# Kernel tuning notes

Hardware: AMD Instinct MI355X
Metric: run time of the kernel (lower is better)

## Reference

```python
import jax, jax.numpy as jnp
import numpy as np


def setup_inputs() -> dict:
    key = jax.random.key(0)
    k1, k2 = jax.random.split(key)
    z = jax.random.normal(k1, (16, 256, 32, 32), dtype=jnp.float32)
    emb = jax.random.normal(k2, (8192, 256), dtype=jnp.float32)
    return {"z": z, "emb": emb}


def reference(z, emb):
    B, C, H, W = z.shape
    # [B,C,H,W] -> [B*H*W, C], distances in fp32 for precision
    z_f = jnp.transpose(z, (0, 2, 3, 1)).reshape(-1, C).astype(jnp.float32)
    e = emb.astype(jnp.float32)
    # squared-distance expansion: ||z||^2 - 2 z.e + ||e||^2  -> [N, K]
    d = (
        jnp.sum(z_f * z_f, axis=1, keepdims=True)
        - 2.0 * (z_f @ e.T)
        + jnp.sum(e * e, axis=1)[None, :]
    )
    idx = jnp.argmin(d, axis=1)  # [N]
    out = emb[idx].astype(z.dtype)  # codebook gather
    return jnp.transpose(out.reshape(B, H, W, C), (0, 3, 1, 2))
```

## Files before the change

kernel.cpp:

```cpp
#include <hip/hip_runtime.h>
#include <stdint.h>

#define NB   16
#define CD   256
#define HW   1024
#define NQ   16384
#define KCN  8192

typedef unsigned long long u64;
typedef unsigned short     u16;
using f32x4  = __attribute__((ext_vector_type(4))) float;
using bf16x8 = __attribute__((ext_vector_type(8))) __bf16;

#define ZTB_OFF  0
#define EMBB_OFF 8388608
#define EH_OFF   12582912
#define CAND_OFF 12615680

static __device__ __forceinline__ void gl_lds16(const void* g, void* l) {
  __builtin_amdgcn_global_load_lds(
      (const __attribute__((address_space(1))) void*)g,
      (__attribute__((address_space(3))) void*)l, 16, 0, 0);
}

static __device__ __forceinline__ unsigned bf16r(float x) {
  unsigned u = __float_as_uint(x);
  return (u + 0x7fffu + ((u >> 16) & 1u)) >> 16;
}

static __device__ __forceinline__ u64 umin64(u64 a, u64 b) { return a < b ? a : b; }
static __device__ __forceinline__ u64 umax64(u64 a, u64 b) { return a < b ? b : a; }

__global__ __launch_bounds__(256) void k_prep(const float* __restrict__ z,
                                              const float* __restrict__ emb,
                                              u16* __restrict__ zTb,
                                              u16* __restrict__ embB,
                                              float* __restrict__ eH) {
  const int bx = (int)blockIdx.x;
  if (bx < 1024) {
    __shared__ float tile[64][65];
    const int b   = bx >> 6;
    const int hwT = (bx >> 2) & 15;
    const int cT  = bx & 3;
    const int tx  = threadIdx.x & 63;
    const int ty  = threadIdx.x >> 6;
    const float* src = z + (size_t)(b * CD + cT * 64) * HW + hwT * 64;
#pragma unroll
    for (int i = 0; i < 16; ++i) {
      const int c_l = ty + 4 * i;
      tile[c_l][tx] = src[(size_t)c_l * HW + tx];
    }
    __syncthreads();
    const size_t dbase = (size_t)(b * HW + hwT * 64) * CD + cT * 64;
#pragma unroll
    for (int i = 0; i < 16; ++i) {
      const int hw_l = ty + 4 * i;
      zTb[dbase + (size_t)hw_l * CD + tx] = (u16)bf16r(tile[tx][hw_l]);
    }
  } else {
    const int wave = (bx - 1024) * 4 + ((int)threadIdx.x >> 6);
    const int lane = threadIdx.x & 63;
#pragma unroll
    for (int it = 0; it < 8; ++it) {
      const int row = wave * 8 + it;
      const float4 v = *(const float4*)(emb + (size_t)row * CD + lane * 4);
      uint2 pk;
      pk.x = bf16r(v.x) | (bf16r(v.y) << 16);
      pk.y = bf16r(v.z) | (bf16r(v.w) << 16);
      *(uint2*)(embB + (size_t)row * CD + lane * 4) = pk;
      float s = v.x * v.x + v.y * v.y + v.z * v.z + v.w * v.w;
#pragma unroll
      for (int off = 32; off; off >>= 1) s += __shfl_xor(s, off, 64);
      if (lane == 0) eH[row] = 0.5f * s + 1024.0f;
    }
  }
}

#define NT  8

__global__ __launch_bounds__(256, 2) void k_argmin(const u16* __restrict__ zTb,
                                                   const u16* __restrict__ embB,
                                                   const float* __restrict__ eH,
                                                   u64* __restrict__ cand) {
  __shared__ __align__(16) u16 As0[128 * 64];
  __shared__ __align__(16) u16 Bs0[128 * 64];
  __shared__ __align__(16) u16 As1[128 * 64];
  __shared__ __align__(16) u16 Bs1[128 * 64];
  const int tid  = threadIdx.x;
  const int w    = tid >> 6;
  const int lane = tid & 63;
  const int l15  = lane & 15, quad = lane >> 4, l7 = lane & 7;
  const int q0    = (int)(blockIdx.x >> 3) * 128;
  const int split = (int)(blockIdx.x & 7);
  const int wq0 = (w & 1) * 64, wn0 = (w >> 1) * 64, wh = w >> 1;

  const int srow  = w * 32 + (lane >> 3);
  const int scol8 = (l7 ^ (lane >> 3)) * 8;
  const int ldsL  = w * 4096 + lane * 16;
  const int co0 = ((0 * 4 + quad) ^ l7) * 16;
  const int co1 = ((1 * 4 + quad) ^ l7) * 16;

  const float FMAX = __uint_as_float(0x7F7FFFFFu);
  float b1[16], b2[16];
#pragma unroll
  for (int s = 0; s < 16; ++s) { b1[s] = FMAX; b2[s] = FMAX; }

  f32x4 acc[4][4];

  {
    const int n0i = split * 1024;
#pragma unroll
    for (int i = 0; i < 4; ++i) {
      const int row = srow + i * 8;
      gl_lds16(zTb  + (size_t)(q0 + row) * CD + 0 * 64 + scol8,
               (char*)As0 + ldsL + i * 1024);
      gl_lds16(embB + (size_t)(n0i + row) * CD + 0 * 64 + scol8,
               (char*)Bs0 + ldsL + i * 1024);
    }
  }
  __syncthreads();

#define KSTEP(PA, PB, NA, NBuf, NKC, NN0)                                            \
  do {                                                                               \
    _Pragma("unroll")                                                                \
    for (int i = 0; i < 4; ++i) {                                                    \
      const int row = srow + i * 8;                                                  \
      gl_lds16(zTb  + (size_t)(q0 + row) * CD + (NKC) * 64 + scol8,                  \
               (char*)NA + ldsL + i * 1024);                                         \
      gl_lds16(embB + (size_t)((NN0) + row) * CD + (NKC) * 64 + scol8,               \
               (char*)NBuf + ldsL + i * 1024);                                       \
    }                                                                                \
    _Pragma("unroll")                                                                \
    for (int ks = 0; ks < 2; ++ks) {                                                 \
      const int co = ks ? co1 : co0;                                                 \
      bf16x8 af[4], bfr[4];                                                          \
      _Pragma("unroll")                                                              \
      for (int i = 0; i < 4; ++i)                                                    \
        af[i] = *(const bf16x8*)((const char*)PA + (wq0 + i * 16 + l15) * 128 + co); \
      _Pragma("unroll")                                                              \
      for (int j = 0; j < 4; ++j)                                                    \
        bfr[j] = *(const bf16x8*)((const char*)PB + (wn0 + j * 16 + l15) * 128 + co);\
      _Pragma("unroll")                                                              \
      for (int i = 0; i < 4; ++i)                                                    \
        _Pragma("unroll")                                                            \
        for (int j = 0; j < 4; ++j)                                                  \
          acc[i][j] = __builtin_amdgcn_mfma_f32_16x16x32_bf16(af[i], bfr[j],         \
                                                              acc[i][j], 0, 0, 0);   \
    }                                                                                \
    __syncthreads();                                                                 \
  } while (0)

  for (int nt = 0; nt < NT; ++nt) {
    const int n0  = split * 1024 + nt * 128;
    const int n0n = (nt == NT - 1) ? n0 : n0 + 128;
    float eh[4];
#pragma unroll
    for (int j = 0; j < 4; ++j) eh[j] = eH[n0 + wn0 + 16 * j + l15];

#pragma unroll
    for (int i = 0; i < 4; ++i)
#pragma unroll
      for (int j = 0; j < 4; ++j) acc[i][j] = f32x4{0.f, 0.f, 0.f, 0.f};

    KSTEP(As0, Bs0, As1, Bs1, 1, n0);
    KSTEP(As1, Bs1, As0, Bs0, 2, n0);
    KSTEP(As0, Bs0, As1, Bs1, 3, n0);
    KSTEP(As1, Bs1, As0, Bs0, 0, n0n);

#pragma unroll
    for (int i = 0; i < 4; ++i) {
#pragma unroll
      for (int r = 0; r < 4; ++r) {
        const int s = i * 4 + r;
        float kq[4];
#pragma unroll
        for (int j = 0; j < 4; ++j) {
          const unsigned kb = (__float_as_uint(eh[j] - acc[i][j][r]) & ~31u)
                              | (unsigned)(nt * 4 + j);
          kq[j] = __uint_as_float(kb);
        }
        const float lo01 = fminf(kq[0], kq[1]), hi01 = fmaxf(kq[0], kq[1]);
        const float lo23 = fminf(kq[2], kq[3]), hi23 = fmaxf(kq[2], kq[3]);
        const float best = fminf(lo01, lo23);
        const float sec  = fminf(fmaxf(lo01, lo23), fminf(hi01, hi23));
        b2[s] = fminf(fmaxf(best, b1[s]), fminf(sec, b2[s]));
        b1[s] = fminf(best, b1[s]);
      }
    }
  }
#undef KSTEP

#pragma unroll
  for (int s = 0; s < 16; ++s) {
    u64 x1 = ((u64)__float_as_uint(b1[s]) << 32) | (unsigned)l15;
    u64 x2 = ((u64)__float_as_uint(b2[s]) << 32) | (unsigned)l15;
#pragma unroll
    for (int off = 1; off < 16; off <<= 1) {
      const u64 o1 = __shfl_xor(x1, off, 64);
      const u64 o2 = __shfl_xor(x2, off, 64);
      const u64 lo = umin64(x1, o1);
      const u64 hi = umax64(x1, o1);
      x1 = lo;
      x2 = umin64(hi, umin64(x2, o2));
    }
    if (l15 == 0) {
      const int i = s >> 2, r = s & 3;
      const int q = q0 + wq0 + i * 16 + quad * 4 + r;
      const unsigned kb1 = (unsigned)(x1 >> 32), kb2 = (unsigned)(x2 >> 32);
      const int n1 = split * 1024 + (int)((kb1 >> 2) & 7) * 128 + wn0
                     + 16 * (int)(kb1 & 3) + (int)(x1 & 15);
      const int n2 = split * 1024 + (int)((kb2 >> 2) & 7) * 128 + wn0
                     + 16 * (int)(kb2 & 3) + (int)(x2 & 15);
      cand[(size_t)q * 32 + split * 4 + wh * 2 + 0] = ((u64)kb1 << 32) | (unsigned)n1;
      cand[(size_t)q * 32 + split * 4 + wh * 2 + 1] = ((u64)kb2 << 32) | (unsigned)n2;
    }
  }
}

__global__ __launch_bounds__(256) void k_pick_out(const float* __restrict__ z,
                                                  const float* __restrict__ emb,
                                                  const u64* __restrict__ cand,
                                                  float* __restrict__ out) {
  __shared__ float zs[16][257];
  __shared__ float tile[16][257];
  const int t    = (int)threadIdx.x;
  const int lane = t & 63;
  const int wv   = t >> 6;
  const int sub  = lane >> 4;
  const int l15  = lane & 15;
  const int q0b  = (int)blockIdx.x * 16;
  const int b    = q0b >> 10, hw0 = q0b & 1023;
  const int q    = q0b + wv * 4 + sub;
  const int hwl  = wv * 4 + sub;

  {
    const float* zp = z + ((size_t)(b * CD + t)) * HW + hw0;
    const float4 a0 = *(const float4*)(zp + 0);
    const float4 a1 = *(const float4*)(zp + 4);
    const float4 a2 = *(const float4*)(zp + 8);
    const float4 a3 = *(const float4*)(zp + 12);
    zs[0][t] = a0.x;  zs[1][t] = a0.y;  zs[2][t] = a0.z;  zs[3][t] = a0.w;
    zs[4][t] = a1.x;  zs[5][t] = a1.y;  zs[6][t] = a1.z;  zs[7][t] = a1.w;
    zs[8][t] = a2.x;  zs[9][t] = a2.y;  zs[10][t] = a2.z; zs[11][t] = a2.w;
    zs[12][t] = a3.x; zs[13][t] = a3.y; zs[14][t] = a3.z; zs[15][t] = a3.w;
  }
  __syncthreads();

  const u64* cp = cand + (size_t)q * 32 + l15 * 2;
  const u64 v0 = cp[0], v1 = cp[1];
  u64 s0 = umin64(v0, v1), s1 = umax64(v0, v1), s2 = ~0ull, s3 = ~0ull;
#pragma unroll
  for (int off = 1; off < 16; off <<= 1) {
    const u64 b0 = __shfl_xor(s0, off, 64);
    const u64 b1 = __shfl_xor(s1, off, 64);
    const u64 b2 = __shfl_xor(s2, off, 64);
    const u64 b3 = __shfl_xor(s3, off, 64);
    const u64 c0 = umin64(s0, b0);
    const u64 c1 = umin64(umin64(s1, b1), umax64(s0, b0));
    const u64 c2 = umin64(umin64(s2, b2),
                          umin64(umax64(s1, b0), umax64(s0, b1)));
    const u64 c3 = umin64(umin64(umin64(s3, b3), umax64(s2, b0)),
                          umin64(umax64(s0, b2), umax64(s1, b1)));
    s0 = c0; s1 = c1; s2 = c2; s3 = c3;
  }
  const u64 sel[4] = {s0, s1, s2, s3};

  float zq[16];
#pragma unroll
  for (int j = 0; j < 16; ++j) zq[j] = zs[hwl][j * 16 + l15];

  double bd = 1e300;
  int bi = 0x7fffffff;
  float keep[16];
#pragma unroll
  for (int j = 0; j < 16; ++j) keep[j] = 0.f;
#pragma unroll
  for (int c4 = 0; c4 < 4; ++c4) {
    const int idx = (int)(unsigned)(sel[c4] & 0xffffffffull);
    const float* er = emb + (size_t)idx * CD;
    float ev[16];
#pragma unroll
    for (int j = 0; j < 16; ++j) ev[j] = er[j * 16 + l15];
    double s = 0.0;
#pragma unroll
    for (int j = 0; j < 16; ++j) {
      const double d = (double)zq[j] - (double)ev[j];
      s += d * d;
    }
#pragma unroll
    for (int off = 1; off < 16; off <<= 1) s += __shfl_xor(s, off, 64);
    const bool better = (s < bd) || (s == bd && idx < bi);
    if (better) {
      bd = s; bi = idx;
#pragma unroll
      for (int j = 0; j < 16; ++j) keep[j] = ev[j];
    }
  }
#pragma unroll
  for (int j = 0; j < 16; ++j) tile[hwl][j * 16 + l15] = keep[j];
  __syncthreads();
  const int cluster = t >> 4;
  const int ll      = t & 15;
  float* obase = out + (size_t)b * CD * HW + hw0 + ll;
#pragma unroll
  for (int j = 0; j < 16; ++j) {
    const int c = 16 * j + cluster;
    obase[(size_t)c * HW] = tile[ll][c];
  }
}

extern "C" void kernel_launch(void* const* d_in, const int* in_sizes, int n_in,
                              void* d_out, int out_size, void* d_ws, size_t ws_size,
                              hipStream_t stream) {
  const float* z   = (const float*)d_in[0];
  const float* emb = (const float*)d_in[1];
  float* out = (float*)d_out;

  char* ws = (char*)d_ws;
  u16*   zTb  = (u16*)(ws + ZTB_OFF);
  u16*   embB = (u16*)(ws + EMBB_OFF);
  float* eH   = (float*)(ws + EH_OFF);
  u64*   cand = (u64*)(ws + CAND_OFF);

  k_prep<<<1280, 256, 0, stream>>>(z, emb, zTb, embB, eH);
  k_argmin<<<1024, 256, 0, stream>>>(zTb, embB, eH, cand);
  k_pick_out<<<1024, 256, 0, stream>>>(z, emb, cand, out);
}
```

Measured before the change: 180.7 us.

## Halve K-chunk to 32 and double occupancy to four blocks per CU

Shrinks each LDS staging tile from 128x64 to 128x32 bf16, which halves shared memory per block, and raises launch bounds to 4 blocks per CU. The swizzle and address math are reworked for the 64-byte rows, and the pipeline now runs 8 half-size K steps per N tile instead of 4. More resident waves can hide load latency, but there are twice as many barriers per tile and a tighter register budget. That budget must hold 64 accumulators plus the 32 running-min registers, so spills are a risk.

```diff
diff --git a/kernel.cpp b/kernel.cpp
--- a/kernel.cpp
+++ b/kernel.cpp
@@ -78,27 +78,32 @@
 
 #define NT  8
 
-__global__ __launch_bounds__(256, 2) void k_argmin(const u16* __restrict__ zTb,
+__global__ __launch_bounds__(256, 4) void k_argmin(const u16* __restrict__ zTb,
                                                    const u16* __restrict__ embB,
                                                    const float* __restrict__ eH,
                                                    u64* __restrict__ cand) {
-  __shared__ __align__(16) u16 As0[128 * 64];
-  __shared__ __align__(16) u16 Bs0[128 * 64];
-  __shared__ __align__(16) u16 As1[128 * 64];
-  __shared__ __align__(16) u16 Bs1[128 * 64];
+  __shared__ __align__(16) u16 As0[128 * 32];
+  __shared__ __align__(16) u16 Bs0[128 * 32];
+  __shared__ __align__(16) u16 As1[128 * 32];
+  __shared__ __align__(16) u16 Bs1[128 * 32];
   const int tid  = threadIdx.x;
   const int w    = tid >> 6;
   const int lane = tid & 63;
-  const int l15  = lane & 15, quad = lane >> 4, l7 = lane & 7;
+  const int l15  = lane & 15, quad = lane >> 4;
   const int q0    = (int)(blockIdx.x >> 3) * 128;
   const int split = (int)(blockIdx.x & 7);
   const int wq0 = (w & 1) * 64, wn0 = (w >> 1) * 64, wh = w >> 1;
 
-  const int srow  = w * 32 + (lane >> 3);
-  const int scol8 = (l7 ^ (lane >> 3)) * 8;
-  const int ldsL  = w * 4096 + lane * 16;
-  const int co0 = ((0 * 4 + quad) ^ l7) * 16;
-  const int co1 = ((1 * 4 + quad) ^ l7) * 16;
+  const int srow = tid >> 2;
+  const int g0   = (tid & 3) ^ ((srow >> 1) & 3);
+  const int ldsD0 = tid * 16;
+  const int ldsD1 = 4096 + tid * 16;
+  const char* aSrcT = (const char*)(zTb + (size_t)(q0 + srow) * CD) + g0 * 16;
+  const char* bSrcT = (const char*)(embB + (size_t)(split * 1024 + srow) * CD) + g0 * 16;
+
+  const int co  = (quad ^ ((l15 >> 1) & 3)) * 16;
+  const int aRd = (wq0 + l15) * 64 + co;
+  const int bRd = (wn0 + l15) * 64 + co;
 
   const float FMAX = __uint_as_float(0x7F7FFFFFu);
   float b1[16], b2[16];
@@ -107,52 +112,37 @@
 
   f32x4 acc[4][4];
 
-  {
-    const int n0i = split * 1024;
-#pragma unroll
-    for (int i = 0; i < 4; ++i) {
-      const int row = srow + i * 8;
-      gl_lds16(zTb  + (size_t)(q0 + row) * CD + 0 * 64 + scol8,
-               (char*)As0 + ldsL + i * 1024);
-      gl_lds16(embB + (size_t)(n0i + row) * CD + 0 * 64 + scol8,
-               (char*)Bs0 + ldsL + i * 1024);
-    }
-  }
+  gl_lds16(aSrcT,         (char*)As0 + ldsD0);
+  gl_lds16(aSrcT + 32768, (char*)As0 + ldsD1);
+  gl_lds16(bSrcT,         (char*)Bs0 + ldsD0);
+  gl_lds16(bSrcT + 32768, (char*)Bs0 + ldsD1);
   __syncthreads();
 
-#define KSTEP(PA, PB, NA, NBuf, NKC, NN0)                                            \
+#define KSTEP(PA, PB, NA, NB, AP, BP)                                                \
   do {                                                                               \
+    gl_lds16((AP),         (char*)(NA) + ldsD0);                                     \
+    gl_lds16((AP) + 32768, (char*)(NA) + ldsD1);                                     \
+    gl_lds16((BP),         (char*)(NB) + ldsD0);                                     \
+    gl_lds16((BP) + 32768, (char*)(NB) + ldsD1);                                     \
+    bf16x8 af[4], bfr[4];                                                            \
     _Pragma("unroll")                                                                \
-    for (int i = 0; i < 4; ++i) {                                                    \
-      const int row = srow + i * 8;                                                  \
-      gl_lds16(zTb  + (size_t)(q0 + row) * CD + (NKC) * 64 + scol8,                  \
-               (char*)NA + ldsL + i * 1024);                                         \
-      gl_lds16(embB + (size_t)((NN0) + row) * CD + (NKC) * 64 + scol8,               \
-               (char*)NBuf + ldsL + i * 1024);                                       \
-    }                                                                                \
+    for (int i = 0; i < 4; ++i)                                                      \
+      af[i] = *(const bf16x8*)((const char*)(PA) + aRd + i * 1024);                  \
     _Pragma("unroll")                                                                \
-    for (int ks = 0; ks < 2; ++ks) {                                                 \
-      const int co = ks ? co1 : co0;                                                 \
-      bf16x8 af[4], bfr[4];                                                          \
-      _Pragma("unroll")                                                              \
-      for (int i = 0; i < 4; ++i)                                                    \
-        af[i] = *(const bf16x8*)((const char*)PA + (wq0 + i * 16 + l15) * 128 + co); \
+    for (int j = 0; j < 4; ++j)                                                      \
+      bfr[j] = *(const bf16x8*)((const char*)(PB) + bRd + j * 1024);                 \
+    _Pragma("unroll")                                                                \
+    for (int i = 0; i < 4; ++i)                                                      \
       _Pragma("unroll")                                                              \
       for (int j = 0; j < 4; ++j)                                                    \
-        bfr[j] = *(const bf16x8*)((const char*)PB + (wn0 + j * 16 + l15) * 128 + co);\
-      _Pragma("unroll")                                                              \
-      for (int i = 0; i < 4; ++i)                                                    \
-        _Pragma("unroll")                                                            \
-        for (int j = 0; j < 4; ++j)                                                  \
-          acc[i][j] = __builtin_amdgcn_mfma_f32_16x16x32_bf16(af[i], bfr[j],         \
-                                                              acc[i][j], 0, 0, 0);   \
-    }                                                                                \
+        acc[i][j] = __builtin_amdgcn_mfma_f32_16x16x32_bf16(af[i], bfr[j],           \
+                                                            acc[i][j], 0, 0, 0);     \
     __syncthreads();                                                                 \
   } while (0)
 
   for (int nt = 0; nt < NT; ++nt) {
-    const int n0  = split * 1024 + nt * 128;
-    const int n0n = (nt == NT - 1) ? n0 : n0 + 128;
+    const int n0 = split * 1024 + nt * 128;
+    const char* bNext = (nt == NT - 1) ? bSrcT : (bSrcT + 65536);
     float eh[4];
 #pragma unroll
     for (int j = 0; j < 4; ++j) eh[j] = eH[n0 + wn0 + 16 * j + l15];
@@ -162,10 +152,14 @@
 #pragma unroll
       for (int j = 0; j < 4; ++j) acc[i][j] = f32x4{0.f, 0.f, 0.f, 0.f};
 
-    KSTEP(As0, Bs0, As1, Bs1, 1, n0);
-    KSTEP(As1, Bs1, As0, Bs0, 2, n0);
-    KSTEP(As0, Bs0, As1, Bs1, 3, n0);
-    KSTEP(As1, Bs1, As0, Bs0, 0, n0n);
+    KSTEP(As0, Bs0, As1, Bs1, aSrcT + 64,  bSrcT + 64);
+    KSTEP(As1, Bs1, As0, Bs0, aSrcT + 128, bSrcT + 128);
+    KSTEP(As0, Bs0, As1, Bs1, aSrcT + 192, bSrcT + 192);
+    KSTEP(As1, Bs1, As0, Bs0, aSrcT + 256, bSrcT + 256);
+    KSTEP(As0, Bs0, As1, Bs1, aSrcT + 320, bSrcT + 320);
+    KSTEP(As1, Bs1, As0, Bs0, aSrcT + 384, bSrcT + 384);
+    KSTEP(As0, Bs0, As1, Bs1, aSrcT + 448, bSrcT + 448);
+    KSTEP(As1, Bs1, As0, Bs0, aSrcT + 0,   bNext);
 
 #pragma unroll
     for (int i = 0; i < 4; ++i) {
@@ -187,6 +181,7 @@
         b1[s] = fminf(best, b1[s]);
       }
     }
+    bSrcT += 65536;
   }
 #undef KSTEP
 
```

Result: slower. 312.4 us (+72.9%).
